# Performance work log

Measured on AMD Instinct MI355X. Metric: run time of the kernel, lower is better.

## Reference

```python
import jax, jax.numpy as jnp
import numpy as np

IN_F = 512
OUT_F = 256
N = 8192
ALPHA = 0.2  # LeakyReLU negative slope
NEG_BIG = -9e15


def setup_inputs() -> dict:
    key = jax.random.key(0)
    k1, k2, k3, k4 = jax.random.split(key, 4)
    x = jax.random.normal(k1, (N, IN_F), dtype=jnp.float32)
    adj = jax.random.randint(k2, (N, N), 0, 2, dtype=jnp.int32)
    # Xavier-uniform-like params
    limW = float(np.sqrt(6.0 / (IN_F + OUT_F)))
    W = jax.random.uniform(k3, (IN_F, OUT_F), jnp.float32, -limW, limW)
    lima = float(np.sqrt(6.0 / (2 * OUT_F + 1)))
    a = jax.random.uniform(k4, (2 * OUT_F, 1), jnp.float32, -lima, lima)
    bias = jnp.zeros((OUT_F,), jnp.float32)
    return {"x": x, "adj": adj, "W": W, "a": a, "bias": bias}


def reference(x, adj, W, a, bias):
    h = x @ W  # (N, OUT_F)
    # Additive attention score e_ij = leakyrelu(a1.h_i + a2.h_j)
    # (same math as the NxNx2F concat in the original, without materializing it)
    a1 = a[:OUT_F, 0]
    a2 = a[OUT_F:, 0]
    s1 = h @ a1  # (N,)
    s2 = h @ a2  # (N,)
    e = jax.nn.leaky_relu(s1[:, None] + s2[None, :], negative_slope=ALPHA)  # (N, N)
    e = jnp.where(adj > 0, e, NEG_BIG)
    attention = jax.nn.softmax(e, axis=1)  # dropout is identity in eval mode
    h_prime = attention @ h + bias
    return h_prime
```

## Files before the change

kernel.cpp:

```cpp
#include <hip/hip_runtime.h>

#define NN 8192
#define INF_ 512
#define OUTF 256
#define LOG2E 1.4426950408889634f

typedef __attribute__((ext_vector_type(8))) short short8;
typedef __attribute__((ext_vector_type(4))) float f4;
typedef __attribute__((ext_vector_type(4))) int i4;

__device__ __forceinline__ unsigned short f2bf(float f) {
  union { float f; unsigned u; } v; v.f = f;
  unsigned r = v.u + 0x7fffu + ((v.u >> 16) & 1u);
  return (unsigned short)(r >> 16);
}
__device__ __forceinline__ float bf2f(unsigned short h) {
  union { unsigned u; float f; } v; v.u = ((unsigned)h) << 16;
  return v.f;
}

__global__ void k_wsplit(const float* __restrict__ W, unsigned short* __restrict__ Whi,
                         unsigned short* __restrict__ Wlo) {
  int idx = blockIdx.x * 256 + threadIdx.x;
  int k = idx >> 8, c = idx & 255;
  float w = W[idx];
  unsigned short hi = f2bf(w);
  unsigned short lo = f2bf(w - bf2f(hi));
  Whi[c * INF_ + k] = hi;
  Wlo[c * INF_ + k] = lo;
}

__global__ void __launch_bounds__(64) k_h(
    const float* __restrict__ x, const float* __restrict__ a,
    const unsigned short* __restrict__ Whi, const unsigned short* __restrict__ Wlo,
    unsigned short* __restrict__ hT, float* __restrict__ s1, float* __restrict__ s2) {
  const int b = blockIdx.x;
  const int rowbase = (b >> 1) * 16;
  const int colbase = (b & 1) * 128;
  const int l = threadIdx.x;
  const int r15 = l & 15, kg = l >> 4;

  f4 acc[8];
#pragma unroll
  for (int i = 0; i < 8; ++i) acc[i] = (f4){0.f, 0.f, 0.f, 0.f};

  for (int kk = 0; kk < INF_; kk += 32) {
    const float* xp = x + (rowbase + r15) * INF_ + kk + kg * 8;
    f4 xa = *(const f4*)xp;
    f4 xb = *(const f4*)(xp + 4);
    short8 ahi, alo;
#pragma unroll
    for (int e = 0; e < 8; ++e) {
      float f = (e < 4) ? xa[e] : xb[e - 4];
      unsigned short h = f2bf(f);
      ahi[e] = (short)h;
      alo[e] = (short)f2bf(f - bf2f(h));
    }
#pragma unroll
    for (int cg = 0; cg < 8; ++cg) {
      int col = colbase + cg * 16 + r15;
      const short8 bhi = *(const short8*)(Whi + col * INF_ + kk + kg * 8);
      const short8 blo = *(const short8*)(Wlo + col * INF_ + kk + kg * 8);
      acc[cg] = __builtin_amdgcn_mfma_f32_16x16x32_bf16(ahi, bhi, acc[cg], 0, 0, 0);
      acc[cg] = __builtin_amdgcn_mfma_f32_16x16x32_bf16(ahi, blo, acc[cg], 0, 0, 0);
      acc[cg] = __builtin_amdgcn_mfma_f32_16x16x32_bf16(alo, bhi, acc[cg], 0, 0, 0);
    }
  }
  float sp1[4] = {0, 0, 0, 0}, sp2[4] = {0, 0, 0, 0};
#pragma unroll
  for (int cg = 0; cg < 8; ++cg) {
    int col = colbase + cg * 16 + r15;
    float a1v = a[col], a2v = a[OUTF + col];
#pragma unroll
    for (int r = 0; r < 4; ++r) {
      float v = acc[cg][r];
      int row = rowbase + kg * 4 + r;
      hT[col * NN + row] = f2bf(v);
      sp1[r] += v * a1v;
      sp2[r] += v * a2v;
    }
  }
#pragma unroll
  for (int r = 0; r < 4; ++r) {
#pragma unroll
    for (int m = 1; m < 16; m <<= 1) {
      sp1[r] += __shfl_xor(sp1[r], m, 16);
      sp2[r] += __shfl_xor(sp2[r], m, 16);
    }
    if (r15 == 0) {
      atomicAdd(&s1[rowbase + kg * 4 + r], sp1[r]);
      atomicAdd(&s2[rowbase + kg * 4 + r], sp2[r]);
    }
  }
}

__global__ void __launch_bounds__(256, 2) k_attn(
    const int* __restrict__ adj, const float* __restrict__ s1G,
    const float* __restrict__ s2G, const unsigned short* __restrict__ hT,
    float* __restrict__ accG, float* __restrict__ lG) {
  __shared__ unsigned short lds[2][8192];
  const int b = blockIdx.x;
  const int chunk = b & 7;
  const int rowblk = b >> 3;
  const int tid = threadIdx.x;
  const int wr = tid >> 6;
  const int l = tid & 63;
  const int r15 = l & 15, kg = l >> 4;
  const int rowbase = rowblk * 128 + wr * 32;
  const int row0 = rowbase + r15;
  const int row1 = rowbase + 16 + r15;
  const int jbase = chunk * 1024;

  const float s1_0 = s1G[row0];
  const float s1_1 = s1G[row1];

  f4 acc[2][16];
#pragma unroll
  for (int g = 0; g < 2; ++g)
#pragma unroll
    for (int c = 0; c < 16; ++c) acc[g][c] = (f4){0.f, 0.f, 0.f, 0.f};
  float lsum0 = 0.f, lsum1 = 0.f;

  const int c_st = wr * 64 + (l >> 2);
  const int s_st = l & 3;

  {
#pragma unroll
    for (int q = 0; q < 4; ++q) {
      int c = c_st + q * 16;
      int kp = (s_st - (c >> 1)) & 3;
      const unsigned short* src = hT + c * NN + jbase + kp * 8;
      unsigned short* dst = &lds[0][(wr * 64 + q * 16) * 32];
      __builtin_amdgcn_global_load_lds(
          (const __attribute__((address_space(1))) unsigned int*)src,
          (__attribute__((address_space(3))) unsigned int*)dst, 16, 0, 0);
    }
  }
  i4 adjb[2][2][2];
  f4 s2b[2][2];
  {
    const int* ap0 = adj + row0 * NN + jbase + kg * 8;
    const int* ap1 = adj + row1 * NN + jbase + kg * 8;
    adjb[0][0][0] = *(const i4*)ap0; adjb[0][0][1] = *(const i4*)(ap0 + 4);
    adjb[0][1][0] = *(const i4*)ap1; adjb[0][1][1] = *(const i4*)(ap1 + 4);
    const float* sp = s2G + jbase + kg * 8;
    s2b[0][0] = *(const f4*)sp; s2b[0][1] = *(const f4*)(sp + 4);
  }
  __syncthreads();

#pragma unroll 2
  for (int t = 0; t < 32; ++t) {
    const int cur = t & 1, nxt = cur ^ 1;
    if (t + 1 < 32) {
      int j0 = jbase + (t + 1) * 32;
#pragma unroll
      for (int q = 0; q < 4; ++q) {
        int c = c_st + q * 16;
        int kp = (s_st - (c >> 1)) & 3;
        const unsigned short* src = hT + c * NN + j0 + kp * 8;
        unsigned short* dst = &lds[nxt][(wr * 64 + q * 16) * 32];
        __builtin_amdgcn_global_load_lds(
            (const __attribute__((address_space(1))) unsigned int*)src,
            (__attribute__((address_space(3))) unsigned int*)dst, 16, 0, 0);
      }
      const int* ap0 = adj + row0 * NN + j0 + kg * 8;
      const int* ap1 = adj + row1 * NN + j0 + kg * 8;
      adjb[nxt][0][0] = *(const i4*)ap0; adjb[nxt][0][1] = *(const i4*)(ap0 + 4);
      adjb[nxt][1][0] = *(const i4*)ap1; adjb[nxt][1][1] = *(const i4*)(ap1 + 4);
      const float* sp = s2G + j0 + kg * 8;
      s2b[nxt][0] = *(const f4*)sp; s2b[nxt][1] = *(const f4*)(sp + 4);
    }
    short8 af0, af1;
#pragma unroll
    for (int e = 0; e < 8; ++e) {
      float sv = (e < 4) ? s2b[cur][0][e] : s2b[cur][1][e - 4];
      int m0 = (e < 4) ? adjb[cur][0][0][e] : adjb[cur][0][1][e - 4];
      int m1 = (e < 4) ? adjb[cur][1][0][e] : adjb[cur][1][1][e - 4];
      float x0 = s1_0 + sv, x1 = s1_1 + sv;
      float lr0 = fmaxf(x0, 0.2f * x0);
      float lr1 = fmaxf(x1, 0.2f * x1);
      float p0 = __builtin_amdgcn_exp2f(lr0 * LOG2E);
      float p1 = __builtin_amdgcn_exp2f(lr1 * LOG2E);
      float w0 = (m0 > 0) ? p0 : 0.0f;
      float w1 = (m1 > 0) ? p1 : 0.0f;
      unsigned short h0 = f2bf(w0), h1 = f2bf(w1);
      af0[e] = (short)h0; af1[e] = (short)h1;
      lsum0 += bf2f(h0);
      lsum1 += bf2f(h1);
    }
#pragma unroll
    for (int cg = 0; cg < 16; ++cg) {
      int c = cg * 16 + r15;
      int slot = (kg + (c >> 1)) & 3;
      const short8 bfrag = *(const short8*)&lds[cur][c * 32 + slot * 8];
      acc[0][cg] = __builtin_amdgcn_mfma_f32_16x16x32_bf16(af0, bfrag, acc[0][cg], 0, 0, 0);
      acc[1][cg] = __builtin_amdgcn_mfma_f32_16x16x32_bf16(af1, bfrag, acc[1][cg], 0, 0, 0);
    }
    __syncthreads();
  }

  lsum0 += __shfl_xor(lsum0, 16, 64);
  lsum0 += __shfl_xor(lsum0, 32, 64);
  lsum1 += __shfl_xor(lsum1, 16, 64);
  lsum1 += __shfl_xor(lsum1, 32, 64);
  if (kg == 0) {
    atomicAdd(&lG[row0], lsum0);
    atomicAdd(&lG[row1], lsum1);
  }
#pragma unroll
  for (int g = 0; g < 2; ++g)
#pragma unroll
    for (int cg = 0; cg < 16; ++cg)
#pragma unroll
      for (int r = 0; r < 4; ++r) {
        int row = rowbase + g * 16 + kg * 4 + r;
        int col = cg * 16 + r15;
        atomicAdd(&accG[row * OUTF + col], acc[g][cg][r]);
      }
}

__global__ void k_final(const float* __restrict__ accG, const float* __restrict__ lG,
                        const float* __restrict__ bias, float* __restrict__ out) {
  int idx = blockIdx.x * 256 + threadIdx.x;
  int row = idx >> 6;
  int c4 = idx & 63;
  f4 v = ((const f4*)accG)[idx];
  float inv = 1.0f / lG[row];
  f4 bb = ((const f4*)bias)[c4];
  f4 o;
#pragma unroll
  for (int e = 0; e < 4; ++e) o[e] = v[e] * inv + bb[e];
  ((f4*)out)[idx] = o;
}

extern "C" void kernel_launch(void* const* d_in, const int* in_sizes, int n_in,
                              void* d_out, int out_size, void* d_ws, size_t ws_size,
                              hipStream_t stream) {
  const float* x = (const float*)d_in[0];
  const int* adj = (const int*)d_in[1];
  const float* W = (const float*)d_in[2];
  const float* a = (const float*)d_in[3];
  const float* bias = (const float*)d_in[4];
  float* out = (float*)d_out;

  char* ws = (char*)d_ws;
  float* accG = (float*)(ws);
  float* lG   = (float*)(ws + 8388608);
  float* s1   = (float*)(ws + 8421376);
  float* s2   = (float*)(ws + 8454144);
  unsigned short* hT  = (unsigned short*)(ws + 8486912);
  unsigned short* Whi = (unsigned short*)(ws + 12681216);
  unsigned short* Wlo = (unsigned short*)(ws + 12943360);

  hipMemsetAsync(accG, 0, 8486912, stream);
  k_wsplit<<<512, 256, 0, stream>>>(W, Whi, Wlo);
  k_h<<<1024, 64, 0, stream>>>(x, a, Whi, Wlo, hT, s1, s2);
  k_attn<<<512, 256, 0, stream>>>(adj, s1, s2, hT, accG, lG);
  k_final<<<2048, 256, 0, stream>>>(accG, lG, bias, out);
}
```

Before: 188.4 us.

## Drop LDS staging in attention kernel and read hT fragments directly per wave

```diff
diff --git a/kernel.cpp b/kernel.cpp
--- a/kernel.cpp
+++ b/kernel.cpp
@@ -70,7 +70,7 @@
 #pragma unroll
   for (int cg = 0; cg < 8; ++cg) {
     int col = colbase + cg * 16 + r15;
-    float a1v = a[col], a2v = a[OUTF + col];
+    float a1v = a[col] * LOG2E, a2v = a[OUTF + col] * LOG2E;
 #pragma unroll
     for (int r = 0; r < 4; ++r) {
       float v = acc[cg][r];
@@ -94,19 +94,16 @@
   }
 }
 
-__global__ void __launch_bounds__(256, 2) k_attn(
+__global__ void __launch_bounds__(64, 2) k_attn(
     const int* __restrict__ adj, const float* __restrict__ s1G,
     const float* __restrict__ s2G, const unsigned short* __restrict__ hT,
     float* __restrict__ accG, float* __restrict__ lG) {
-  __shared__ unsigned short lds[2][8192];
   const int b = blockIdx.x;
   const int chunk = b & 7;
   const int rowblk = b >> 3;
-  const int tid = threadIdx.x;
-  const int wr = tid >> 6;
-  const int l = tid & 63;
+  const int l = threadIdx.x;
   const int r15 = l & 15, kg = l >> 4;
-  const int rowbase = rowblk * 128 + wr * 32;
+  const int rowbase = rowblk * 32;
   const int row0 = rowbase + r15;
   const int row1 = rowbase + 16 + r15;
   const int jbase = chunk * 1024;
@@ -114,73 +111,49 @@
   const float s1_0 = s1G[row0];
   const float s1_1 = s1G[row1];
 
-  f4 acc[2][16];
-#pragma unroll
-  for (int g = 0; g < 2; ++g)
-#pragma unroll
-    for (int c = 0; c < 16; ++c) acc[g][c] = (f4){0.f, 0.f, 0.f, 0.f};
+  f4 acc0[16], acc1[16];
+#pragma unroll
+  for (int c = 0; c < 16; ++c) {
+    acc0[c] = (f4){0.f, 0.f, 0.f, 0.f};
+    acc1[c] = (f4){0.f, 0.f, 0.f, 0.f};
+  }
   float lsum0 = 0.f, lsum1 = 0.f;
 
-  const int c_st = wr * 64 + (l >> 2);
-  const int s_st = l & 3;
-
-  {
-#pragma unroll
-    for (int q = 0; q < 4; ++q) {
-      int c = c_st + q * 16;
-      int kp = (s_st - (c >> 1)) & 3;
-      const unsigned short* src = hT + c * NN + jbase + kp * 8;
-      unsigned short* dst = &lds[0][(wr * 64 + q * 16) * 32];
-      __builtin_amdgcn_global_load_lds(
-          (const __attribute__((address_space(1))) unsigned int*)src,
-          (__attribute__((address_space(3))) unsigned int*)dst, 16, 0, 0);
-    }
-  }
-  i4 adjb[2][2][2];
-  f4 s2b[2][2];
+  i4 A00, A01, A10, A11;
+  f4 S0, S1;
   {
     const int* ap0 = adj + row0 * NN + jbase + kg * 8;
     const int* ap1 = adj + row1 * NN + jbase + kg * 8;
-    adjb[0][0][0] = *(const i4*)ap0; adjb[0][0][1] = *(const i4*)(ap0 + 4);
-    adjb[0][1][0] = *(const i4*)ap1; adjb[0][1][1] = *(const i4*)(ap1 + 4);
+    A00 = *(const i4*)ap0; A01 = *(const i4*)(ap0 + 4);
+    A10 = *(const i4*)ap1; A11 = *(const i4*)(ap1 + 4);
     const float* sp = s2G + jbase + kg * 8;
-    s2b[0][0] = *(const f4*)sp; s2b[0][1] = *(const f4*)(sp + 4);
-  }
-  __syncthreads();
-
-#pragma unroll 2
+    S0 = *(const f4*)sp; S1 = *(const f4*)(sp + 4);
+  }
+
   for (int t = 0; t < 32; ++t) {
-    const int cur = t & 1, nxt = cur ^ 1;
-    if (t + 1 < 32) {
-      int j0 = jbase + (t + 1) * 32;
-#pragma unroll
-      for (int q = 0; q < 4; ++q) {
-        int c = c_st + q * 16;
-        int kp = (s_st - (c >> 1)) & 3;
-        const unsigned short* src = hT + c * NN + j0 + kp * 8;
-        unsigned short* dst = &lds[nxt][(wr * 64 + q * 16) * 32];
-        __builtin_amdgcn_global_load_lds(
-            (const __attribute__((address_space(1))) unsigned int*)src,
-            (__attribute__((address_space(3))) unsigned int*)dst, 16, 0, 0);
-      }
-      const int* ap0 = adj + row0 * NN + j0 + kg * 8;
-      const int* ap1 = adj + row1 * NN + j0 + kg * 8;
-      adjb[nxt][0][0] = *(const i4*)ap0; adjb[nxt][0][1] = *(const i4*)(ap0 + 4);
-      adjb[nxt][1][0] = *(const i4*)ap1; adjb[nxt][1][1] = *(const i4*)(ap1 + 4);
-      const float* sp = s2G + j0 + kg * 8;
-      s2b[nxt][0] = *(const f4*)sp; s2b[nxt][1] = *(const f4*)(sp + 4);
-    }
+    i4 nA00, nA01, nA10, nA11;
+    f4 nS0, nS1;
+    if (t < 31) {
+      const int jn = jbase + (t + 1) * 32;
+      const int* ap0 = adj + row0 * NN + jn + kg * 8;
+      const int* ap1 = adj + row1 * NN + jn + kg * 8;
+      nA00 = *(const i4*)ap0; nA01 = *(const i4*)(ap0 + 4);
+      nA10 = *(const i4*)ap1; nA11 = *(const i4*)(ap1 + 4);
+      const float* sp = s2G + jn + kg * 8;
+      nS0 = *(const f4*)sp; nS1 = *(const f4*)(sp + 4);
+    }
+
     short8 af0, af1;
 #pragma unroll
     for (int e = 0; e < 8; ++e) {
-      float sv = (e < 4) ? s2b[cur][0][e] : s2b[cur][1][e - 4];
-      int m0 = (e < 4) ? adjb[cur][0][0][e] : adjb[cur][0][1][e - 4];
-      int m1 = (e < 4) ? adjb[cur][1][0][e] : adjb[cur][1][1][e - 4];
+      float sv = (e < 4) ? S0[e] : S1[e - 4];
+      int m0 = (e < 4) ? A00[e] : A01[e - 4];
+      int m1 = (e < 4) ? A10[e] : A11[e - 4];
       float x0 = s1_0 + sv, x1 = s1_1 + sv;
       float lr0 = fmaxf(x0, 0.2f * x0);
       float lr1 = fmaxf(x1, 0.2f * x1);
-      float p0 = __builtin_amdgcn_exp2f(lr0 * LOG2E);
-      float p1 = __builtin_amdgcn_exp2f(lr1 * LOG2E);
+      float p0 = __builtin_amdgcn_exp2f(lr0);
+      float p1 = __builtin_amdgcn_exp2f(lr1);
       float w0 = (m0 > 0) ? p0 : 0.0f;
       float w1 = (m1 > 0) ? p1 : 0.0f;
       unsigned short h0 = f2bf(w0), h1 = f2bf(w1);
@@ -188,15 +161,17 @@
       lsum0 += bf2f(h0);
       lsum1 += bf2f(h1);
     }
+
+    const unsigned short* bp = hT + jbase + t * 32 + kg * 8;
 #pragma unroll
     for (int cg = 0; cg < 16; ++cg) {
-      int c = cg * 16 + r15;
-      int slot = (kg + (c >> 1)) & 3;
-      const short8 bfrag = *(const short8*)&lds[cur][c * 32 + slot * 8];
-      acc[0][cg] = __builtin_amdgcn_mfma_f32_16x16x32_bf16(af0, bfrag, acc[0][cg], 0, 0, 0);
-      acc[1][cg] = __builtin_amdgcn_mfma_f32_16x16x32_bf16(af1, bfrag, acc[1][cg], 0, 0, 0);
-    }
-    __syncthreads();
+      const short8 bfrag = *(const short8*)(bp + (cg * 16 + r15) * NN);
+      acc0[cg] = __builtin_amdgcn_mfma_f32_16x16x32_bf16(af0, bfrag, acc0[cg], 0, 0, 0);
+      acc1[cg] = __builtin_amdgcn_mfma_f32_16x16x32_bf16(af1, bfrag, acc1[cg], 0, 0, 0);
+    }
+
+    A00 = nA00; A01 = nA01; A10 = nA10; A11 = nA11;
+    S0 = nS0; S1 = nS1;
   }
 
   lsum0 += __shfl_xor(lsum0, 16, 64);
@@ -208,15 +183,13 @@
     atomicAdd(&lG[row1], lsum1);
   }
 #pragma unroll
-  for (int g = 0; g < 2; ++g)
-#pragma unroll
-    for (int cg = 0; cg < 16; ++cg)
-#pragma unroll
-      for (int r = 0; r < 4; ++r) {
-        int row = rowbase + g * 16 + kg * 4 + r;
-        int col = cg * 16 + r15;
-        atomicAdd(&accG[row * OUTF + col], acc[g][cg][r]);
-      }
+  for (int cg = 0; cg < 16; ++cg)
+#pragma unroll
+    for (int r = 0; r < 4; ++r) {
+      int col = cg * 16 + r15;
+      atomicAdd(&accG[(rowbase + kg * 4 + r) * OUTF + col], acc0[cg][r]);
+      atomicAdd(&accG[(rowbase + 16 + kg * 4 + r) * OUTF + col], acc1[cg][r]);
+    }
 }
 
 __global__ void k_final(const float* __restrict__ accG, const float* __restrict__ lG,
@@ -255,6 +228,6 @@
   hipMemsetAsync(accG, 0, 8486912, stream);
   k_wsplit<<<512, 256, 0, stream>>>(W, Whi, Wlo);
   k_h<<<1024, 64, 0, stream>>>(x, a, Whi, Wlo, hT, s1, s2);
-  k_attn<<<512, 256, 0, stream>>>(adj, s1, s2, hT, accG, lG);
+  k_attn<<<2048, 64, 0, stream>>>(adj, s1, s2, hT, accG, lG);
   k_final<<<2048, 256, 0, stream>>>(accG, lG, bias, out);
 }
```

Result: slower. 267.0 us (+41.7%).
